# Kernel tuning notes

Hardware: AMD Instinct MI355X
Metric: run time of the kernel (lower is better)

## Reference

```python
import jax, jax.numpy as jnp
import numpy as np

D_MODEL = 768
DT_RANK = D_MODEL // 16  # 48
D_CONV = 4
D_INNER = 2 * D_MODEL    # 1536
D_STATE = 16
BATCH, SEQ_LEN = 1, 4096


def setup_inputs() -> dict:
    key = jax.random.key(0)
    ks = jax.random.split(key, 11)
    def n(k, shape, scale=0.02):
        return jax.random.normal(k, shape, dtype=jnp.float32) * scale
    return {
        "u": jax.random.normal(ks[0], (BATCH, SEQ_LEN, D_MODEL), dtype=jnp.float32),
        "in_proj_w": n(ks[1], (2 * D_INNER, D_MODEL)),
        "conv_w": n(ks[2], (D_INNER, 1, D_CONV)),
        "conv_b": n(ks[3], (D_INNER,)),
        "x_dt_w": n(ks[4], (DT_RANK, D_INNER)),
        "x_b_w": n(ks[5], (D_STATE, D_INNER)),
        "x_c_w": n(ks[6], (D_STATE, D_INNER)),
        "dt_w": n(ks[7], (D_INNER, DT_RANK)),
        "dt_b": n(ks[8], (D_INNER,)),
        # HF Mamba-style S4D-real init: A_log = log(1..N) per channel
        "A_log": jnp.log(jnp.tile(jnp.arange(1, D_STATE + 1, dtype=jnp.float32), (D_INNER, 1))),
        "D_param": jnp.ones((D_INNER,), dtype=jnp.float32),
        "out_proj_w": n(ks[9], (D_MODEL, D_INNER)),
    }


def _silu(x):
    return x * jax.nn.sigmoid(x)


def reference(u, in_proj_w, conv_w, conv_b, x_dt_w, x_b_w, x_c_w,
              dt_w, dt_b, A_log, D_param, out_proj_w):
    batch = u.shape[0]
    # input projection -> x, z  [B, L, D_INNER] each
    xz = u @ in_proj_w.T
    x, z = jnp.split(xz, 2, axis=-1)
    # causal depthwise conv1d over time
    x_ncl = jnp.transpose(x, (0, 2, 1))  # [B, D_INNER, L]
    x_conv = jax.lax.conv_general_dilated(
        x_ncl, conv_w, window_strides=(1,), padding=[(D_CONV - 1, 0)],
        dimension_numbers=("NCH", "OIH", "NCH"), feature_group_count=D_INNER)
    x_conv = x_conv + conv_b[None, :, None]
    x_conv = _silu(jnp.transpose(x_conv, (0, 2, 1)))  # [B, L, D_INNER]
    # data-dependent SSM parameters
    dt_rank = x_conv @ x_dt_w.T                      # [B, L, DT_RANK]
    Bm = x_conv @ x_b_w.T                            # [B, L, D_STATE]
    Cm = x_conv @ x_c_w.T                            # [B, L, D_STATE]
    dt = jax.nn.softplus(dt_rank @ dt_w.T + dt_b)    # [B, L, D_INNER]
    A = -jnp.exp(A_log)                              # [D_INNER, D_STATE]
    dA = jnp.exp(dt[..., None] * A)                  # [B, L, D_INNER, D_STATE]
    dB = dt[..., None] * Bm[:, :, None, :]           # [B, L, D_INNER, D_STATE]

    def step(h, inp):
        dA_t, dB_t, x_t, C_t = inp
        h = h * dA_t + x_t[..., None] * dB_t                 # [B, D_INNER, D_STATE]
        y_t = jnp.sum(h * C_t[:, None, :], axis=-1) + D_param * x_t
        return h, y_t

    h0 = jnp.zeros((batch, D_INNER, D_STATE), dtype=u.dtype)
    scan_inputs = (jnp.moveaxis(dA, 1, 0), jnp.moveaxis(dB, 1, 0),
                   jnp.moveaxis(x_conv, 1, 0), jnp.moveaxis(Cm, 1, 0))
    _, y_ssm = jax.lax.scan(step, h0, scan_inputs)   # [L, B, D_INNER]
    y = jnp.moveaxis(y_ssm, 0, 1) * _silu(z)         # [B, L, D_INNER]
    return y @ out_proj_w.T                          # [B, L, D_MODEL]
```

## Files before the change

### kernel.cpp

```cpp
#include <hip/hip_runtime.h>
#include <math.h>

#define L      4096
#define DM     768
#define DI     1536
#define DS     16
#define DR     48
#define NCOMB  80
#define CH     32
#define NC     128
#define G2_S   16
#define G2_KC  96
#define XZROW  6144

typedef unsigned short u16;
typedef unsigned int   u32;
typedef __attribute__((ext_vector_type(8))) short bf16x8;
typedef __attribute__((ext_vector_type(4))) float f32x4;

__device__ __forceinline__ float silu_f(float v) { return v / (1.f + __expf(-v)); }

__device__ __forceinline__ u16 f2bf(float f) {
    u32 u = __float_as_uint(f);
    return (u16)((u + 0x7fffu + ((u >> 16) & 1u)) >> 16);
}
__device__ __forceinline__ float bf2f(u16 h) {
    return __uint_as_float(((u32)h) << 16);
}

__device__ __forceinline__ void gl_lds16(const u16* g, u16* l) {
    __builtin_amdgcn_global_load_lds(
        (const __attribute__((address_space(1))) void*)g,
        (__attribute__((address_space(3))) void*)l, 16, 0, 0);
}

__global__ __launch_bounds__(256)
void gemm_bf16_bt(const u16* __restrict__ A, const u16* __restrict__ W,
                  float* __restrict__ C, int M, int N, int K)
{
    __shared__ u16 As[2][128 * 32];
    __shared__ u16 Bs[2][128 * 32];

    const int tid  = threadIdx.x;
    const int lane = tid & 63;
    const int wave = tid >> 6;
    const int wr   = (wave >> 1) * 64;
    const int wc   = (wave & 1) * 64;
    const int m0   = blockIdx.y * 128;
    const int n0   = blockIdx.x * 128;

    const int r0 = tid >> 2;
    const int k0 = (tid & 3) * 8;

    const int frow = lane & 15;
    const int fk   = (lane >> 4) * 8;

    f32x4 acc[4][4];
    #pragma unroll
    for (int i = 0; i < 4; ++i)
        #pragma unroll
        for (int j = 0; j < 4; ++j)
            acc[i][j] = (f32x4){0.f, 0.f, 0.f, 0.f};

    const int NT = K >> 5;

#define STAGE(buf, kk) {                                                       \
        const u16* ga = A + (size_t)(m0 + r0) * K + (kk) + k0;                 \
        const u16* gw = W + (size_t)(n0 + r0) * K + (kk) + k0;                 \
        gl_lds16(ga,                   &As[buf][tid * 8]);                     \
        gl_lds16(ga + (size_t)64 * K,  &As[buf][2048 + tid * 8]);              \
        gl_lds16(gw,                   &Bs[buf][tid * 8]);                     \
        gl_lds16(gw + (size_t)64 * K,  &Bs[buf][2048 + tid * 8]); }

    STAGE(0, 0);
    __syncthreads();

    for (int t = 0; t < NT; ++t) {
        const int b = t & 1;
        if (t + 1 < NT) STAGE(b ^ 1, (t + 1) << 5);

        bf16x8 af[4], bw[4];
        #pragma unroll
        for (int m = 0; m < 4; ++m)
            af[m] = *(const bf16x8*)&As[b][(wr + m * 16 + frow) * 32 + fk];
        #pragma unroll
        for (int n = 0; n < 4; ++n)
            bw[n] = *(const bf16x8*)&Bs[b][(wc + n * 16 + frow) * 32 + fk];

        #pragma unroll
        for (int m = 0; m < 4; ++m)
            #pragma unroll
            for (int n = 0; n < 4; ++n)
                acc[m][n] = __builtin_amdgcn_mfma_f32_16x16x32_bf16(
                    af[m], bw[n], acc[m][n], 0, 0, 0);

        __syncthreads();
    }
#undef STAGE

    const int crow = (lane >> 4) * 4;
    const int ccol = lane & 15;
    #pragma unroll
    for (int m = 0; m < 4; ++m)
        #pragma unroll
        for (int n = 0; n < 4; ++n)
            #pragma unroll
            for (int r = 0; r < 4; ++r)
                C[(size_t)(m0 + wr + m * 16 + crow + r) * N
                  + n0 + wc + n * 16 + ccol] = acc[m][n][r];
}

__global__ __launch_bounds__(256)
void gemm_bf16_bt_n64(const u16* __restrict__ A, int lda,
                      const u16* __restrict__ W, int ldw,
                      float* __restrict__ C, int M, int N, int K)
{
    __shared__ u16 As[2][128 * 32];
    __shared__ u16 Bs[2][64 * 32];

    const int tid  = threadIdx.x;
    const int lane = tid & 63;
    const int wave = tid >> 6;
    const int wr   = (wave >> 1) * 64;
    const int wc   = (wave & 1) * 32;
    const int m0   = blockIdx.y * 128;
    const int n0   = blockIdx.x * 64;

    const int r0 = tid >> 2;
    const int k0 = (tid & 3) * 8;

    const int frow = lane & 15;
    const int fk   = (lane >> 4) * 8;

    f32x4 acc[4][2];
    #pragma unroll
    for (int i = 0; i < 4; ++i)
        #pragma unroll
        for (int j = 0; j < 2; ++j)
            acc[i][j] = (f32x4){0.f, 0.f, 0.f, 0.f};

    const int NT = K >> 5;

#define STG(buf, kk) {                                                         \
        const u16* ga = A + (size_t)(m0 + r0) * lda + (kk) + k0;               \
        gl_lds16(ga,                     &As[buf][tid * 8]);                   \
        gl_lds16(ga + (size_t)64 * lda,  &As[buf][2048 + tid * 8]);            \
        gl_lds16(W + (size_t)(n0 + r0) * ldw + (kk) + k0, &Bs[buf][tid * 8]); }

    STG(0, 0);
    __syncthreads();

    for (int t = 0; t < NT; ++t) {
        const int b = t & 1;
        if (t + 1 < NT) STG(b ^ 1, (t + 1) << 5);

        bf16x8 af[4], bw[2];
        #pragma unroll
        for (int m = 0; m < 4; ++m)
            af[m] = *(const bf16x8*)&As[b][(wr + m * 16 + frow) * 32 + fk];
        #pragma unroll
        for (int n = 0; n < 2; ++n)
            bw[n] = *(const bf16x8*)&Bs[b][(wc + n * 16 + frow) * 32 + fk];

        #pragma unroll
        for (int m = 0; m < 4; ++m)
            #pragma unroll
            for (int n = 0; n < 2; ++n)
                acc[m][n] = __builtin_amdgcn_mfma_f32_16x16x32_bf16(
                    af[m], bw[n], acc[m][n], 0, 0, 0);

        __syncthreads();
    }
#undef STG

    const int crow = (lane >> 4) * 4;
    const int ccol = lane & 15;
    #pragma unroll
    for (int m = 0; m < 4; ++m)
        #pragma unroll
        for (int n = 0; n < 2; ++n)
            #pragma unroll
            for (int r = 0; r < 4; ++r)
                C[(size_t)(m0 + wr + m * 16 + crow + r) * N
                  + n0 + wc + n * 16 + ccol] = acc[m][n][r];
}

#define NU4  (L * DM / 4)
#define NW4  (2 * DI * DM / 4)
#define NWT  (DI * NCOMB)
__global__ __launch_bounds__(256)
void pack_early_k(const float* __restrict__ u, const float* __restrict__ Wip,
                  const float* __restrict__ xdt, const float* __restrict__ xb,
                  const float* __restrict__ xc,
                  u16* __restrict__ ubf, u16* __restrict__ Wipb,
                  float* __restrict__ Wt)
{
    int i = blockIdx.x * 256 + threadIdx.x;
    if (i < NU4) {
        const float4 v = ((const float4*)u)[i];
        ushort4 o; o.x = f2bf(v.x); o.y = f2bf(v.y); o.z = f2bf(v.z); o.w = f2bf(v.w);
        ((ushort4*)ubf)[i] = o;
        return;
    }
    i -= NU4;
    if (i < NW4) {
        const float4 v = ((const float4*)Wip)[i];
        ushort4 o; o.x = f2bf(v.x); o.y = f2bf(v.y); o.z = f2bf(v.z); o.w = f2bf(v.w);
        ((ushort4*)Wipb)[i] = o;
        return;
    }
    i -= NW4;
    if (i < NWT) {
        const int k = i / NCOMB, n = i - k * NCOMB;
        float v;
        if (n < 48)      v = xdt[n * DI + k];
        else if (n < 64) v = xb[(n - 48) * DI + k];
        else             v = xc[(n - 64) * DI + k];
        Wt[i] = v;
    }
}

#define NO4  (DM * DI / 4)
__global__ __launch_bounds__(256)
void pack_wop_k(const float* __restrict__ Wop, u16* __restrict__ xzu)
{
    int i = blockIdx.x * 256 + threadIdx.x;
    if (i >= NO4) return;
    const float4 v = ((const float4*)Wop)[i];
    ushort4 o; o.x = f2bf(v.x); o.y = f2bf(v.y); o.z = f2bf(v.z); o.w = f2bf(v.w);
    const int e = i * 4;
    const int r = e / DI, c = e - r * DI;
    *(ushort4*)(xzu + (size_t)r * XZROW + 1536 + c) = o;
}

__global__ __launch_bounds__(256)
void conv_silu_v4(const float* __restrict__ xz, const float* __restrict__ cw,
                  const float* __restrict__ cb, float* __restrict__ xcv)
{
    int idx = blockIdx.x * 256 + threadIdx.x;
    if (idx >= L * (DI / 4)) return;
    const int t = idx / (DI / 4);
    const int q = idx - t * (DI / 4);
    const int d = q * 4;

    const float4 w0 = ((const float4*)cw)[d + 0];
    const float4 w1 = ((const float4*)cw)[d + 1];
    const float4 w2 = ((const float4*)cw)[d + 2];
    const float4 w3 = ((const float4*)cw)[d + 3];
    float4 acc = ((const float4*)cb)[q];

    const float* base = xz + d;
    #pragma unroll
    for (int j = 0; j < 4; ++j) {
        const int tt = t - 3 + j;
        if (tt >= 0) {
            const float4 x = *(const float4*)(base + (size_t)tt * (2 * DI));
            acc.x = fmaf(((const float*)&w0)[j], x.x, acc.x);
            acc.y = fmaf(((const float*)&w1)[j], x.y, acc.y);
            acc.z = fmaf(((const float*)&w2)[j], x.z, acc.z);
            acc.w = fmaf(((const float*)&w3)[j], x.w, acc.w);
        }
    }
    float4 o;
    o.x = silu_f(acc.x); o.y = silu_f(acc.y);
    o.z = silu_f(acc.z); o.w = silu_f(acc.w);
    ((float4*)xcv)[idx] = o;
}

__global__ __launch_bounds__(256)
void gemm2_splitk(const float* __restrict__ A, const float* __restrict__ Wt,
                  float* __restrict__ part)
{
    __shared__ float As[G2_KC][65];
    __shared__ float Ws[G2_KC][80];

    const int tid  = threadIdx.x;
    const int m0   = blockIdx.x * 64;
    const int koff = blockIdx.y * G2_KC;

    {
        const int r = tid >> 2, cg = tid & 3;
        #pragma unroll
        for (int j = 0; j < 6; ++j) {
            const int kk = (j * 4 + cg) * 4;
            const float4 v = *(const float4*)(A + (size_t)(m0 + r) * DI + koff + kk);
            As[kk + 0][r] = v.x; As[kk + 1][r] = v.y;
            As[kk + 2][r] = v.z; As[kk + 3][r] = v.w;
        }
    }
    for (int i = tid; i < G2_KC * 80; i += 256)
        (&Ws[0][0])[i] = Wt[(size_t)koff * 80 + i];
    __syncthreads();

    const int g  = tid >> 6;
    const int r  = tid & 63;
    const int c0 = g * 20;

    float acc[20];
    #pragma unroll
    for (int j = 0; j < 20; ++j) acc[j] = 0.f;

    #pragma unroll 2
    for (int k = 0; k < G2_KC; ++k) {
        const float a = As[k][r];
        #pragma unroll
        for (int q = 0; q < 5; ++q) {
            const float4 w = *(const float4*)&Ws[k][c0 + q * 4];
            acc[q * 4 + 0] = fmaf(a, w.x, acc[q * 4 + 0]);
            acc[q * 4 + 1] = fmaf(a, w.y, acc[q * 4 + 1]);
            acc[q * 4 + 2] = fmaf(a, w.z, acc[q * 4 + 2]);
            acc[q * 4 + 3] = fmaf(a, w.w, acc[q * 4 + 3]);
        }
    }

    float* p = part + (size_t)blockIdx.y * (L * NCOMB)
                    + (size_t)(m0 + r) * NCOMB + c0;
    #pragma unroll
    for (int q = 0; q < 5; ++q)
        ((float4*)p)[q] = make_float4(acc[q * 4], acc[q * 4 + 1],
                                      acc[q * 4 + 2], acc[q * 4 + 3]);
}

__global__ __launch_bounds__(256)
void gemm2_reduce(const float* __restrict__ part, float* __restrict__ dtbc)
{
    int i = blockIdx.x * 256 + threadIdx.x;
    if (i >= L * NCOMB) return;
    float s = 0.f;
    #pragma unroll
    for (int j = 0; j < G2_S; ++j)
        s += part[(size_t)j * L * NCOMB + i];
    dtbc[i] = s;
}

__global__ __launch_bounds__(256)
void dt_k(const float* __restrict__ dtbc, const float* __restrict__ dtw,
          const float* __restrict__ dtb, float* __restrict__ dt)
{
    __shared__ float dtr_s[32][48];
    const int tid = threadIdx.x;
    const int d   = blockIdx.x * 256 + tid;
    const int t0  = blockIdx.y * 32;

    for (int i = tid; i < 384; i += 256) {
        const int r = i / 12, c = (i - r * 12) * 4;
        const float4 v = *(const float4*)(dtbc + (size_t)(t0 + r) * NCOMB + c);
        *(float4*)&dtr_s[r][c] = v;
    }
    __syncthreads();

    float w[48];
    #pragma unroll
    for (int j = 0; j < 12; ++j) {
        const float4 v = *(const float4*)(dtw + (size_t)d * DR + j * 4);
        w[j * 4 + 0] = v.x; w[j * 4 + 1] = v.y;
        w[j * 4 + 2] = v.z; w[j * 4 + 3] = v.w;
    }
    const float b = dtb[d];

    for (int t = 0; t < 32; ++t) {
        float s = b;
        #pragma unroll
        for (int j = 0; j < 12; ++j) {
            const float4 v = *(const float4*)&dtr_s[t][j * 4];
            s = fmaf(v.x, w[j * 4 + 0], s);
            s = fmaf(v.y, w[j * 4 + 1], s);
            s = fmaf(v.z, w[j * 4 + 2], s);
            s = fmaf(v.w, w[j * 4 + 3], s);
        }
        dt[(size_t)(t0 + t) * DI + d] = (s > 20.f) ? s : log1pf(expf(s));
    }
}

__global__ __launch_bounds__(256)
void scan1_k(const float* __restrict__ dt, const float* __restrict__ xcv,
             const float* __restrict__ dtbc, const float* __restrict__ alog,
             u16* __restrict__ hloc, float* __restrict__ Ssum)
{
    __shared__ float Bs[CH][DS];
    const int c = blockIdx.y;
    const int d = blockIdx.x * 256 + threadIdx.x;

    for (int i = threadIdx.x; i < CH * DS; i += 256) {
        int tt = i >> 4, n = i & 15;
        Bs[tt][n] = dtbc[(size_t)(c * CH + tt) * NCOMB + 48 + n];
    }
    __syncthreads();

    float Ad[DS], h[DS];
    #pragma unroll
    for (int n = 0; n < DS; ++n) {
        Ad[n] = -expf(alog[d * DS + n]);
        h[n] = 0.f;
    }

    size_t base = (size_t)(c * CH) * DI + d;
    float S = 0.f;
    for (int tt = 0; tt < CH; ++tt, base += DI) {
        const float dtv = dt[base];
        const float xv  = xcv[base];
        S += dtv;
        const float xdt = xv * dtv;
        #pragma unroll
        for (int n = 0; n < DS; ++n)
            h[n] = fmaf(h[n], __expf(Ad[n] * dtv), xdt * Bs[tt][n]);
    }

    u16* o = hloc + ((size_t)c * DI + d) * DS;
    #pragma unroll
    for (int q = 0; q < 4; ++q) {
        ushort4 pk;
        pk.x = f2bf(h[q * 4 + 0]); pk.y = f2bf(h[q * 4 + 1]);
        pk.z = f2bf(h[q * 4 + 2]); pk.w = f2bf(h[q * 4 + 3]);
        *(ushort4*)(o + q * 4) = pk;
    }
    Ssum[c * DI + d] = S;
}

__global__ __launch_bounds__(256)
void scan2_k(u16* hc, const float* __restrict__ Ssum,
             const float* __restrict__ alog)
{
    const int p = blockIdx.x * 256 + threadIdx.x;
    if (p >= DI * DS) return;
    const int d = p >> 4;
    const float Ad = -expf(alog[p]);
    float h = 0.f;
    for (int c = 0; c < NC; ++c) {
        const size_t o = (size_t)c * DI * DS + p;
        const float hl = bf2f(hc[o]);
        hc[o] = f2bf(h);
        h = fmaf(h, __expf(Ad * Ssum[c * DI + d]), hl);
    }
}

__global__ __launch_bounds__(256)
void scan3_k(const float* __restrict__ dt, const float* __restrict__ xcv,
             const float* __restrict__ dtbc, const float* __restrict__ alog,
             const u16* __restrict__ carry, const float* __restrict__ Dp,
             const float* __restrict__ xz, u16* __restrict__ ybf)
{
    __shared__ float Bs[CH][DS];
    __shared__ float Cs[CH][DS];
    const int c = blockIdx.y;
    const int d = blockIdx.x * 256 + threadIdx.x;

    for (int i = threadIdx.x; i < CH * DS; i += 256) {
        int tt = i >> 4, n = i & 15;
        Bs[tt][n] = dtbc[(size_t)(c * CH + tt) * NCOMB + 48 + n];
        Cs[tt][n] = dtbc[(size_t)(c * CH + tt) * NCOMB + 64 + n];
    }
    __syncthreads();

    float Ad[DS], h[DS];
    const u16* co = carry + ((size_t)c * DI + d) * DS;
    #pragma unroll
    for (int q = 0; q < 4; ++q) {
        const ushort4 cv = *(const ushort4*)(co + q * 4);
        h[q * 4 + 0] = bf2f(cv.x); h[q * 4 + 1] = bf2f(cv.y);
        h[q * 4 + 2] = bf2f(cv.z); h[q * 4 + 3] = bf2f(cv.w);
    }
    #pragma unroll
    for (int n = 0; n < DS; ++n)
        Ad[n] = -expf(alog[d * DS + n]);
    const float Dv = Dp[d];

    int t = c * CH;
    for (int tt = 0; tt < CH; ++tt, ++t) {
        const size_t o = (size_t)t * DI + d;
        const float dtv = dt[o];
        const float xv  = xcv[o];
        const float xdt = xv * dtv;
        float y = Dv * xv;
        #pragma unroll
        for (int n = 0; n < DS; ++n) {
            h[n] = fmaf(h[n], __expf(Ad[n] * dtv), xdt * Bs[tt][n]);
            y = fmaf(h[n], Cs[tt][n], y);
        }
        const float z = xz[(size_t)t * (2 * DI) + DI + d];
        ybf[(size_t)t * XZROW + d] = f2bf(y * silu_f(z));
    }
}

extern "C" void kernel_launch(void* const* d_in, const int* in_sizes, int n_in,
                              void* d_out, int out_size, void* d_ws, size_t ws_size,
                              hipStream_t stream)
{
    const float* u    = (const float*)d_in[0];
    const float* Wip  = (const float*)d_in[1];
    const float* cw   = (const float*)d_in[2];
    const float* cb   = (const float*)d_in[3];
    const float* xdt  = (const float*)d_in[4];
    const float* xbw  = (const float*)d_in[5];
    const float* xcw  = (const float*)d_in[6];
    const float* dtw  = (const float*)d_in[7];
    const float* dtb  = (const float*)d_in[8];
    const float* alog = (const float*)d_in[9];
    const float* Dp   = (const float*)d_in[10];
    const float* Wop  = (const float*)d_in[11];
    float* out = (float*)d_out;

    float* ws   = (float*)d_ws;
    float* xz   = ws;
    float* xcv  = xz   + (size_t)L * 2 * DI;
    float* dtbc = xcv  + (size_t)L * DI;
    float* dty  = dtbc + (size_t)L * NCOMB;
    float* Wt   = dty  + (size_t)L * DI;
    u16*   hc   = (u16*)(Wt + (size_t)DI * NCOMB);
    float* Ssum = Wt + (size_t)DI * NCOMB
                     + (size_t)NC * DI * DS / 2;

    u16*   ubf  = (u16*)xcv;
    u16*   Wipb = (u16*)xcv + (size_t)L * DM;
    float* g2p  = dty;
    u16*   xzu  = (u16*)xz;

    const dim3 blk(256);

    pack_early_k<<<(NU4 + NW4 + NWT + 255) / 256, blk, 0, stream>>>(
        u, Wip, xdt, xbw, xcw, ubf, Wipb, Wt);

    gemm_bf16_bt<<<dim3((2 * DI) / 128, L / 128), blk, 0, stream>>>(
        ubf, Wipb, xz, L, 2 * DI, DM);

    conv_silu_v4<<<(L * (DI / 4) + 255) / 256, blk, 0, stream>>>(xz, cw, cb, xcv);

    pack_wop_k<<<(NO4 + 255) / 256, blk, 0, stream>>>(Wop, xzu);

    gemm2_splitk<<<dim3(L / 64, G2_S), blk, 0, stream>>>(xcv, Wt, g2p);
    gemm2_reduce<<<(L * NCOMB + 255) / 256, blk, 0, stream>>>(g2p, dtbc);

    dt_k<<<dim3(DI / 256, L / 32), blk, 0, stream>>>(dtbc, dtw, dtb, dty);

    scan1_k<<<dim3(DI / 256, NC), blk, 0, stream>>>(dty, xcv, dtbc, alog, hc, Ssum);
    scan2_k<<<(DI * DS) / 256, blk, 0, stream>>>(hc, Ssum, alog);
    scan3_k<<<dim3(DI / 256, NC), blk, 0, stream>>>(
        dty, xcv, dtbc, alog, hc, Dp, xz, xzu);

    gemm_bf16_bt_n64<<<dim3(DM / 64, L / 128), blk, 0, stream>>>(
        xzu, XZROW, xzu + 1536, XZROW, out, L, DM, DI);
}
```

Baseline: 240.2 us.

## Halve scan chunk length and store dt as bf16

The chunked scan now uses 16-step chunks with 256 chunks instead of 32 and 128. This doubles the number of blocks in scan1 and scan3, but scan2 runs twice as many serial steps and there is more carry storage. dt is now written by dt_k as bf16 and read as bf16 in both scan passes, which halves that traffic at some cost in precision. The B/C shared-memory fill becomes a single assignment per thread, since CH*DS now equals 256. The hc/Ssum workspace offsets still use NC, so the carry buffer grows.

```diff
diff --git a/kernel.cpp b/kernel.cpp
--- a/kernel.cpp
+++ b/kernel.cpp
@@ -7,8 +7,8 @@
 #define DS     16
 #define DR     48
 #define NCOMB  80
-#define CH     32
-#define NC     128
+#define CH     16
+#define NC     256
 #define G2_S   16
 #define G2_KC  96
 #define XZROW  6144
@@ -26,6 +26,10 @@
 }
 __device__ __forceinline__ float bf2f(u16 h) {
     return __uint_as_float(((u32)h) << 16);
+}
+
+__device__ __forceinline__ float softplus_f(float s) {
+    return (s > 20.f) ? s : log1pf(expf(s));
 }
 
 __device__ __forceinline__ void gl_lds16(const u16* g, u16* l) {
@@ -335,7 +339,7 @@
 
 __global__ __launch_bounds__(256)
 void dt_k(const float* __restrict__ dtbc, const float* __restrict__ dtw,
-          const float* __restrict__ dtb, float* __restrict__ dt)
+          const float* __restrict__ dtb, u16* __restrict__ dt)
 {
     __shared__ float dtr_s[32][48];
     const int tid = threadIdx.x;
@@ -368,12 +372,12 @@
             s = fmaf(v.z, w[j * 4 + 2], s);
             s = fmaf(v.w, w[j * 4 + 3], s);
         }
-        dt[(size_t)(t0 + t) * DI + d] = (s > 20.f) ? s : log1pf(expf(s));
-    }
-}
-
-__global__ __launch_bounds__(256)
-void scan1_k(const float* __restrict__ dt, const float* __restrict__ xcv,
+        dt[(size_t)(t0 + t) * DI + d] = f2bf(softplus_f(s));
+    }
+}
+
+__global__ __launch_bounds__(256)
+void scan1_k(const u16* __restrict__ dt, const float* __restrict__ xcv,
              const float* __restrict__ dtbc, const float* __restrict__ alog,
              u16* __restrict__ hloc, float* __restrict__ Ssum)
 {
@@ -381,8 +385,9 @@
     const int c = blockIdx.y;
     const int d = blockIdx.x * 256 + threadIdx.x;
 
-    for (int i = threadIdx.x; i < CH * DS; i += 256) {
-        int tt = i >> 4, n = i & 15;
+    {
+        const int i = threadIdx.x;
+        const int tt = i >> 4, n = i & 15;
         Bs[tt][n] = dtbc[(size_t)(c * CH + tt) * NCOMB + 48 + n];
     }
     __syncthreads();
@@ -397,7 +402,7 @@
     size_t base = (size_t)(c * CH) * DI + d;
     float S = 0.f;
     for (int tt = 0; tt < CH; ++tt, base += DI) {
-        const float dtv = dt[base];
+        const float dtv = bf2f(dt[base]);
         const float xv  = xcv[base];
         S += dtv;
         const float xdt = xv * dtv;
@@ -435,7 +440,7 @@
 }
 
 __global__ __launch_bounds__(256)
-void scan3_k(const float* __restrict__ dt, const float* __restrict__ xcv,
+void scan3_k(const u16* __restrict__ dt, const float* __restrict__ xcv,
              const float* __restrict__ dtbc, const float* __restrict__ alog,
              const u16* __restrict__ carry, const float* __restrict__ Dp,
              const float* __restrict__ xz, u16* __restrict__ ybf)
@@ -445,8 +450,9 @@
     const int c = blockIdx.y;
     const int d = blockIdx.x * 256 + threadIdx.x;
 
-    for (int i = threadIdx.x; i < CH * DS; i += 256) {
-        int tt = i >> 4, n = i & 15;
+    {
+        const int i = threadIdx.x;
+        const int tt = i >> 4, n = i & 15;
         Bs[tt][n] = dtbc[(size_t)(c * CH + tt) * NCOMB + 48 + n];
         Cs[tt][n] = dtbc[(size_t)(c * CH + tt) * NCOMB + 64 + n];
     }
@@ -468,7 +474,7 @@
     int t = c * CH;
     for (int tt = 0; tt < CH; ++tt, ++t) {
         const size_t o = (size_t)t * DI + d;
-        const float dtv = dt[o];
+        const float dtv = bf2f(dt[o]);
         const float xv  = xcv[o];
         const float xdt = xv * dtv;
         float y = Dv * xv;
@@ -513,6 +519,7 @@
     u16*   ubf  = (u16*)xcv;
     u16*   Wipb = (u16*)xcv + (size_t)L * DM;
     float* g2p  = dty;
+    u16*   dtbf = (u16*)dty;
     u16*   xzu  = (u16*)xz;
 
     const dim3 blk(256);
@@ -530,12 +537,13 @@
     gemm2_splitk<<<dim3(L / 64, G2_S), blk, 0, stream>>>(xcv, Wt, g2p);
     gemm2_reduce<<<(L * NCOMB + 255) / 256, blk, 0, stream>>>(g2p, dtbc);
 
-    dt_k<<<dim3(DI / 256, L / 32), blk, 0, stream>>>(dtbc, dtw, dtb, dty);
-
-    scan1_k<<<dim3(DI / 256, NC), blk, 0, stream>>>(dty, xcv, dtbc, alog, hc, Ssum);
+    dt_k<<<dim3(DI / 256, L / 32), blk, 0, stream>>>(dtbc, dtw, dtb, dtbf);
+
+    scan1_k<<<dim3(DI / 256, NC), blk, 0, stream>>>(
+        dtbf, xcv, dtbc, alog, hc, Ssum);
     scan2_k<<<(DI * DS) / 256, blk, 0, stream>>>(hc, Ssum, alog);
     scan3_k<<<dim3(DI / 256, NC), blk, 0, stream>>>(
-        dty, xcv, dtbc, alog, hc, Dp, xz, xzu);
+        dtbf, xcv, dtbc, alog, hc, Dp, xz, xzu);
 
     gemm_bf16_bt_n64<<<dim3(DM / 64, L / 128), blk, 0, stream>>>(
         xzu, XZROW, xzu + 1536, XZROW, out, L, DM, DI);
```

New measurement: 247.9 us. 1.03x slower.
